# Optimization experiments

Hardware: AMD Instinct MI355X
Metric: run time of the kernel (lower is better)

The kernel has to match this reference:

```python
import jax, jax.numpy as jnp
import numpy as np

B, DIM, H, W = 8, 256, 128, 128
P = 4               # patch_size
HEADS = 8
HD = DIM // HEADS   # head dim = 32
CPB_HIDDEN = 512    # hidden width of the dynamic RPE MLP


def setup_inputs() -> dict:
    key = jax.random.key(0)
    ks = jax.random.split(key, 12)
    s = 0.02
    return {
        "x": jax.random.normal(ks[0], (B, DIM, H, W), dtype=jnp.float32),
        # PatchEmbed2d: Conv2d(dim, dim, kernel=P, stride=P)  weight [O, I, P, P]
        "w_embed": jax.random.normal(ks[1], (DIM, DIM, P, P), dtype=jnp.float32) * s,
        "b_embed": jnp.zeros((DIM,), dtype=jnp.float32),
        # DynamicPosEncoder: MLP(2 -> CPB_HIDDEN -> HEADS) on relative coords
        "cpb_w1": jax.random.normal(ks[2], (CPB_HIDDEN, 2), dtype=jnp.float32) * s,
        "cpb_b1": jnp.zeros((CPB_HIDDEN,), dtype=jnp.float32),
        "cpb_w2": jax.random.normal(ks[3], (HEADS, CPB_HIDDEN), dtype=jnp.float32) * s,
        # MaskAttention2d
        "w_qkv": jax.random.normal(ks[4], (3 * DIM, DIM), dtype=jnp.float32) * s,
        "b_qkv": jnp.zeros((3 * DIM,), dtype=jnp.float32),
        "w_proj": jax.random.normal(ks[5], (DIM, DIM), dtype=jnp.float32) * s,
        "b_proj": jnp.zeros((DIM,), dtype=jnp.float32),
        # PatchUnEmbed2d: ConvTranspose2d(dim, dim, kernel=P, stride=P)  weight [I, O, P, P]
        "w_unembed": jax.random.normal(ks[6], (DIM, DIM, P, P), dtype=jnp.float32) * s,
        "b_unembed": jnp.zeros((DIM,), dtype=jnp.float32),
    }


def _rpe_bias(Hp, Wp, cpb_w1, cpb_b1, cpb_w2):
    """Dynamic relative position bias -> [HEADS, N, N], N = Hp*Wp."""
    # continuous relative-coordinate table [(2Hp-1)*(2Wp-1), 2], normalized to [-1, 1]
    rh = (jnp.arange(2 * Hp - 1, dtype=jnp.float32) - (Hp - 1)) / max(Hp - 1, 1)
    rw = (jnp.arange(2 * Wp - 1, dtype=jnp.float32) - (Wp - 1)) / max(Wp - 1, 1)
    rel = jnp.stack(jnp.meshgrid(rh, rw, indexing="ij"), axis=-1).reshape(-1, 2)
    table = jax.nn.relu(rel @ cpb_w1.T + cpb_b1) @ cpb_w2.T  # [(2Hp-1)(2Wp-1), HEADS]
    # static relative position index [N, N]
    ch = np.arange(Hp)
    cw = np.arange(Wp)
    coords = np.stack(np.meshgrid(ch, cw, indexing="ij")).reshape(2, -1)  # [2, N]
    d = coords[:, :, None] - coords[:, None, :]                           # [2, N, N]
    idx = (d[0] + Hp - 1) * (2 * Wp - 1) + (d[1] + Wp - 1)               # [N, N]
    bias = table[jnp.asarray(idx)]                                        # [N, N, HEADS]
    return bias.transpose(2, 0, 1)                                        # [HEADS, N, N]


def reference(x, w_embed, b_embed, cpb_w1, cpb_b1, cpb_w2,
              w_qkv, b_qkv, w_proj, b_proj, w_unembed, b_unembed):
    Bx, C, Hf, Wf = x.shape
    Hp, Wp = Hf // P, Wf // P
    N = Hp * Wp
    # ---- patch embed: Conv2d(k=P, s=P) as block reshape + einsum ----
    xr = x.reshape(Bx, C, Hp, P, Wp, P)
    z = jnp.einsum("bchpwq,ocpq->bohw", xr, w_embed) + b_embed[None, :, None, None]
    # ---- dynamic RPE bias ----
    bias = _rpe_bias(Hp, Wp, cpb_w1, cpb_b1, cpb_w2)  # [HEADS, N, N]
    # ---- multi-head self-attention over the Hp*Wp grid ----
    tok = z.reshape(Bx, C, N).transpose(0, 2, 1)                     # [B, N, C]
    qkv = tok @ w_qkv.T + b_qkv                                       # [B, N, 3C]
    qkv = qkv.reshape(Bx, N, 3, HEADS, HD).transpose(2, 0, 3, 1, 4)   # [3, B, H, N, hd]
    q, k, v = qkv[0], qkv[1], qkv[2]
    scale = HD ** -0.5
    attn = jnp.einsum("bhnd,bhmd->bhnm", q * scale, k) + bias[None]   # [B, H, N, N]
    attn = jax.nn.softmax(attn, axis=-1)
    out = jnp.einsum("bhnm,bhmd->bhnd", attn, v)                      # [B, H, N, hd]
    out = out.transpose(0, 2, 1, 3).reshape(Bx, N, C)
    out = out @ w_proj.T + b_proj                                     # [B, N, C]
    z2 = out.transpose(0, 2, 1).reshape(Bx, C, Hp, Wp)
    # ---- patch unembed: ConvTranspose2d(k=P, s=P) as einsum + block reshape ----
    y = jnp.einsum("bchw,copq->bohpwq", z2, w_unembed)
    y = y.reshape(Bx, C, Hf, Wf) + b_unembed[None, :, None, None]
    return y
```

## Files before the change

kernel.cpp:

```cpp
#include <hip/hip_runtime.h>
#include <cstdint>
#include <cstddef>


typedef __bf16 bf16x8 __attribute__((ext_vector_type(8)));
typedef float f32x4 __attribute__((ext_vector_type(4)));
typedef unsigned short u16x4 __attribute__((ext_vector_type(4)));

__device__ __forceinline__ unsigned short f2bf(float f) {
  unsigned u = __builtin_bit_cast(unsigned, f);
  u += 0x7fffu + ((u >> 16) & 1u);
  return (unsigned short)(u >> 16);
}
__device__ __forceinline__ float bf2f(unsigned short u) {
  return __builtin_bit_cast(float, ((unsigned)u) << 16);
}

__device__ __forceinline__ void async_ld16(const void* g, void* l) {
  __builtin_amdgcn_global_load_lds(
      (const __attribute__((address_space(1))) void*)g,
      (__attribute__((address_space(3))) void*)l, 16, 0, 0);
}

__device__ __forceinline__ void cvt8_store(unsigned short* dst, float4 a,
                                           float4 b) {
  unsigned short t[8] = {f2bf(a.x), f2bf(a.y), f2bf(a.z), f2bf(a.w),
                         f2bf(b.x), f2bf(b.y), f2bf(b.z), f2bf(b.w)};
  *(uint4*)dst = *(const uint4*)t;
}

__global__ __launch_bounds__(256) void rpe_table_kernel(
    const float* __restrict__ w1, const float* __restrict__ b1,
    const float* __restrict__ w2, float* __restrict__ tableT) {
  int t = blockIdx.x * 256 + threadIdx.x;
  if (t >= 3969) return;
  int a = t / 63, c = t - a * 63;
  float rh = (float)(a - 31) * (1.0f / 31.0f);
  float rw = (float)(c - 31) * (1.0f / 31.0f);
  float acc[8];
#pragma unroll
  for (int h = 0; h < 8; h++) acc[h] = 0.f;
  for (int j = 0; j < 512; j++) {
    float hv = fmaxf(rh * w1[2 * j] + rw * w1[2 * j + 1] + b1[j], 0.f);
#pragma unroll
    for (int h = 0; h < 8; h++) acc[h] += hv * w2[h * 512 + j];
  }
#pragma unroll
  for (int h = 0; h < 8; h++) tableT[h * 4096 + t] = acc[h];
}

__global__ __launch_bounds__(256) void cvt_bf16_kernel(
    const float* __restrict__ src, unsigned short* __restrict__ dst, int n8) {
  int i = blockIdx.x * 256 + threadIdx.x;
  if (i >= n8) return;
  const float4* s4 = (const float4*)src + (size_t)i * 2;
  float4 a = s4[0], b = s4[1];
  unsigned short t[8] = {f2bf(a.x), f2bf(a.y), f2bf(a.z), f2bf(a.w),
                         f2bf(b.x), f2bf(b.y), f2bf(b.z), f2bf(b.w)};
  *(uint4*)(dst + (size_t)i * 8) = *(const uint4*)t;
}

__global__ __launch_bounds__(256) void transpose_cvt_kernel(
    const float* __restrict__ src, unsigned short* __restrict__ dst) {
  __shared__ float tile[32][33];
  int bx = blockIdx.x;
  int by = blockIdx.y;
  int tx = threadIdx.x & 31, ty = threadIdx.x >> 5;
#pragma unroll
  for (int r = 0; r < 32; r += 8)
    tile[ty + r][tx] = src[(size_t)(by * 32 + ty + r) * 4096 + bx * 32 + tx];
  __syncthreads();
#pragma unroll
  for (int r = 0; r < 32; r += 8)
    dst[(size_t)(bx * 32 + ty + r) * 256 + by * 32 + tx] = f2bf(tile[tx][ty + r]);
}

__global__ __launch_bounds__(256) void splitk_reduce_kernel(
    const float* __restrict__ part, const float* __restrict__ bias,
    unsigned short* __restrict__ out) {
  size_t i = ((size_t)blockIdx.x * 256 + threadIdx.x) * 8;
  const float4* p = (const float4*)(part + i);
  const size_t s4 = 2097152 / 4;
  float4 a0 = p[0], a1 = p[1];
#pragma unroll
  for (int s = 1; s < 4; s++) {
    float4 b0 = p[s * s4], b1 = p[s * s4 + 1];
    a0.x += b0.x; a0.y += b0.y; a0.z += b0.z; a0.w += b0.w;
    a1.x += b1.x; a1.y += b1.y; a1.z += b1.z; a1.w += b1.w;
  }
  int col = (int)(i & 255);
  unsigned short t8[8] = {
      f2bf(a0.x + bias[col + 0]), f2bf(a0.y + bias[col + 1]),
      f2bf(a0.z + bias[col + 2]), f2bf(a0.w + bias[col + 3]),
      f2bf(a1.x + bias[col + 4]), f2bf(a1.y + bias[col + 5]),
      f2bf(a1.z + bias[col + 6]), f2bf(a1.w + bias[col + 7])};
  *(uint4*)(out + i) = *(const uint4*)t8;
}

__global__ __launch_bounds__(256) void gemm_embed_kernel(
    const float* __restrict__ x, const unsigned short* __restrict__ B,
    float* __restrict__ Cpart) {
  __shared__ unsigned short As[2 * 128 * 32];
  __shared__ unsigned short Bs[2 * 128 * 32];
  int tid = threadIdx.x;
  int lane = tid & 63, wave = tid >> 6;

  int L = blockIdx.x;
  int xcd = L & 7, j = L >> 3;
  int pair = xcd * 32 + (j >> 1);
  int n0 = (j & 1) * 128;
  int z = pair & 3, y = pair >> 2;
  int m0 = y * 128;
  int wm = (wave & 1) * 64, wn = (wave >> 1) * 64;
  int fr = lane & 15, fh = lane >> 4;

  f32x4 acc[4][4];
#pragma unroll
  for (int i = 0; i < 4; i++)
#pragma unroll
    for (int jj = 0; jj < 4; jj++) acc[i][jj] = (f32x4){0.f, 0.f, 0.f, 0.f};

  int f0 = tid, f1 = tid + 256;
  const unsigned short* Bg0 =
      B + (size_t)(n0 + (f0 >> 2)) * 4096 + z * 1024 + (f0 & 3) * 8;
  const unsigned short* Bg1 =
      B + (size_t)(n0 + (f1 >> 2)) * 4096 + z * 1024 + (f1 & 3) * 8;
  unsigned short* Bl0 = Bs + f0 * 8;
  unsigned short* Bl1 = Bs + f1 * 8;

  const float4* x4 = (const float4*)x;
  int r0 = f0 >> 2, ch0 = f0 & 3;
  int m_0 = m0 + r0, b_0 = m_0 >> 10, hp0 = (m_0 >> 5) & 31, wp0 = m_0 & 31;
  int k_0 = z * 1024 + ch0 * 8, c_0 = k_0 >> 4, p_0 = (k_0 >> 2) & 3;
  const float4* xp0 =
      x4 + (size_t)((b_0 * 256 + c_0) * 128 + hp0 * 4 + p_0) * 32 + wp0;
  int r1 = f1 >> 2, ch1 = f1 & 3;
  int m_1 = m0 + r1, b_1 = m_1 >> 10, hp1 = (m_1 >> 5) & 31, wp1 = m_1 & 31;
  int k_1 = z * 1024 + ch1 * 8, c_1 = k_1 >> 4, p_1 = (k_1 >> 2) & 3;
  const float4* xp1 =
      x4 + (size_t)((b_1 * 256 + c_1) * 128 + hp1 * 4 + p_1) * 32 + wp1;
  unsigned short* Al0 = As + f0 * 8;
  unsigned short* Al1 = As + f1 * 8;

  float4 a00 = xp0[0], a01 = xp0[32], a10 = xp1[0], a11 = xp1[32];
  xp0 += 8192; xp1 += 8192;
  async_ld16(Bg0, Bl0);
  async_ld16(Bg1, Bl1);
  cvt8_store(Al0, a00, a01);
  cvt8_store(Al1, a10, a11);
  __syncthreads();

  for (int t = 0; t < 32; t++) {
    int cur = (t & 1) << 12, nxt = cur ^ 4096;
    if (t < 31) {
      a00 = xp0[0]; a01 = xp0[32]; a10 = xp1[0]; a11 = xp1[32];
      xp0 += 8192; xp1 += 8192;
      int kn = (t + 1) << 5;
      async_ld16(Bg0 + kn, Bl0 + nxt);
      async_ld16(Bg1 + kn, Bl1 + nxt);
    }
    const unsigned short* Asc = As + cur;
    const unsigned short* Bsc = Bs + cur;
    bf16x8 af[4], bfr[4];
#pragma unroll
    for (int tt = 0; tt < 4; tt++) {
      af[tt] = *(const bf16x8*)(Asc + (wm + tt * 16 + fr) * 32 + fh * 8);
      bfr[tt] = *(const bf16x8*)(Bsc + (wn + tt * 16 + fr) * 32 + fh * 8);
    }
#pragma unroll
    for (int mt = 0; mt < 4; mt++)
#pragma unroll
      for (int nt = 0; nt < 4; nt++)
        acc[mt][nt] = __builtin_amdgcn_mfma_f32_16x16x32_bf16(
            af[mt], bfr[nt], acc[mt][nt], 0, 0, 0);
    if (t < 31) {
      cvt8_store(Al0 + nxt, a00, a01);
      cvt8_store(Al1 + nxt, a10, a11);
    }
    __syncthreads();
  }

  float* Cp = Cpart + (size_t)z * 2097152;
#pragma unroll
  for (int mt = 0; mt < 4; mt++) {
    int row0 = m0 + wm + mt * 16 + fh * 4;
#pragma unroll
    for (int nt = 0; nt < 4; nt++) {
      int col = n0 + wn + nt * 16 + fr;
#pragma unroll
      for (int r = 0; r < 4; r++)
        Cp[(size_t)(row0 + r) * 256 + col] = acc[mt][nt][r];
    }
  }
}

template <int CMODE>
__global__ __launch_bounds__(256) void gemm_mfma_kernel(
    const unsigned short* __restrict__ A, const unsigned short* __restrict__ B,
    const float* __restrict__ bias, void* __restrict__ Cv,
    int M, int N, int K, int lda, int ldb, int ldc) {
  __shared__ unsigned short As[2 * 128 * 32];
  __shared__ unsigned short Bs[2 * 128 * 32];
  int tid = threadIdx.x;
  int lane = tid & 63;
  int wave = tid >> 6;
  int m0 = blockIdx.y * 128, n0 = blockIdx.x * 128;
  int wm = (wave & 1) * 64, wn = (wave >> 1) * 64;

  if (CMODE == 4) {
    int s = blockIdx.z;
    A += (size_t)s * K;
    B += (size_t)s * K;
    Cv = (void*)((float*)Cv + (size_t)s * M * N);
  }

  f32x4 acc[4][4];
#pragma unroll
  for (int i = 0; i < 4; i++)
#pragma unroll
    for (int j = 0; j < 4; j++) acc[i][j] = (f32x4){0.f, 0.f, 0.f, 0.f};

  int f0 = tid, f1 = tid + 256;
  const unsigned short* Ag0 = A + (size_t)(m0 + (f0 >> 2)) * lda + (f0 & 3) * 8;
  const unsigned short* Ag1 = A + (size_t)(m0 + (f1 >> 2)) * lda + (f1 & 3) * 8;
  const unsigned short* Bg0 = B + (size_t)(n0 + (f0 >> 2)) * ldb + (f0 & 3) * 8;
  const unsigned short* Bg1 = B + (size_t)(n0 + (f1 >> 2)) * ldb + (f1 & 3) * 8;
  unsigned short* Al0 = As + f0 * 8;
  unsigned short* Al1 = As + f1 * 8;
  unsigned short* Bl0 = Bs + f0 * 8;
  unsigned short* Bl1 = Bs + f1 * 8;

  int fr = lane & 15;
  int fh = lane >> 4;

  int ntiles = K >> 5;
  async_ld16(Ag0, Al0);
  async_ld16(Ag1, Al1);
  async_ld16(Bg0, Bl0);
  async_ld16(Bg1, Bl1);
  __syncthreads();

  for (int t = 0; t < ntiles; t++) {
    int cur = (t & 1) << 12;
    int nxt = cur ^ 4096;
    if (t + 1 < ntiles) {
      int kn = (t + 1) << 5;
      async_ld16(Ag0 + kn, Al0 + nxt);
      async_ld16(Ag1 + kn, Al1 + nxt);
      async_ld16(Bg0 + kn, Bl0 + nxt);
      async_ld16(Bg1 + kn, Bl1 + nxt);
    }
    const unsigned short* Asc = As + cur;
    const unsigned short* Bsc = Bs + cur;
    bf16x8 af[4], bfr[4];
#pragma unroll
    for (int tt = 0; tt < 4; tt++) {
      af[tt] = *(const bf16x8*)(Asc + (wm + tt * 16 + fr) * 32 + fh * 8);
      bfr[tt] = *(const bf16x8*)(Bsc + (wn + tt * 16 + fr) * 32 + fh * 8);
    }
#pragma unroll
    for (int mt = 0; mt < 4; mt++)
#pragma unroll
      for (int nt = 0; nt < 4; nt++)
        acc[mt][nt] = __builtin_amdgcn_mfma_f32_16x16x32_bf16(
            af[mt], bfr[nt], acc[mt][nt], 0, 0, 0);
    __syncthreads();
  }

#pragma unroll
  for (int mt = 0; mt < 4; mt++) {
    int row0 = m0 + wm + mt * 16 + fh * 4;
    if (CMODE == 2) {
      int b = row0 >> 10, hp = (row0 >> 5) & 31, wp = row0 & 31;
      size_t rowoff0 = (size_t)b * 4194304 + hp * 512 + wp * 4;
      float* y = (float*)Cv;
#pragma unroll
      for (int nt = 0; nt < 4; nt++) {
        int col = n0 + wn + nt * 16 + fr;
        int o = col >> 4, p = (col >> 2) & 3, q = col & 3;
        size_t coloff = (size_t)o * 16384 + p * 128 + q;
        float bv = bias[o];
#pragma unroll
        for (int r = 0; r < 4; r++)
          y[rowoff0 + r * 4 + coloff] = acc[mt][nt][r] + bv;
      }
    } else if (CMODE == 3) {
      unsigned short* base = (unsigned short*)Cv;
#pragma unroll
      for (int nt = 0; nt < 4; nt++) {
        int col = n0 + wn + nt * 16 + fr;
        int which = col >> 8, hh = (col >> 5) & 7, d = col & 31;
        float bv = bias[col];
#pragma unroll
        for (int r = 0; r < 4; r++) {
          int row = row0 + r;
          int bb = row >> 10, nn = row & 1023;
          int bh = bb * 8 + hh;
          float v = acc[mt][nt][r] + bv;
          if (which == 0) v *= 0.17677669529663687f;
          size_t addr;
          if (which < 2)
            addr = (size_t)which * 2097152 + ((size_t)bh * 1024 + nn) * 32 + d;
          else
            addr = (size_t)2 * 2097152 + (size_t)bh * 32768 + (size_t)d * 1024 + nn;
          base[addr] = f2bf(v);
        }
      }
    } else if (CMODE == 4) {
      float* Cp = (float*)Cv;
#pragma unroll
      for (int nt = 0; nt < 4; nt++) {
        int col = n0 + wn + nt * 16 + fr;
#pragma unroll
        for (int r = 0; r < 4; r++)
          Cp[(size_t)(row0 + r) * ldc + col] = acc[mt][nt][r];
      }
    } else {
#pragma unroll
      for (int nt = 0; nt < 4; nt++) {
        int col = n0 + wn + nt * 16 + fr;
        float bv = bias ? bias[col] : 0.f;
        unsigned short* C = (unsigned short*)Cv;
#pragma unroll
        for (int r = 0; r < 4; r++)
          C[(size_t)(row0 + r) * ldc + col] = f2bf(acc[mt][nt][r] + bv);
      }
    }
  }
}

__global__ __launch_bounds__(512) void attn_mfma_kernel(
    const unsigned short* __restrict__ Qb, const unsigned short* __restrict__ Kb,
    const unsigned short* __restrict__ Vtb,
    const float* __restrict__ tableT,
    unsigned short* __restrict__ out) {
  __shared__ float th[3972];
  __shared__ unsigned short Ps[2][8][1088];

  int tid = threadIdx.x;
  int lane = tid & 63, w = tid >> 6;
  int n = lane & 15, g = lane >> 4;
  int blk = blockIdx.x;
  int h = blk & 7, b = (blk >> 3) & 7, qt = blk >> 6;
  int bh = b * 8 + h;
  int q0 = qt * 128;

  const unsigned short* Qg = Qb + ((size_t)bh * 1024 + q0) * 32;
  const unsigned short* Kg = Kb + (size_t)bh * 1024 * 32;
  const unsigned short* Vg = Vtb + (size_t)bh * 32 * 1024;
  const float* tg = tableT + (size_t)h * 4096;

  for (int i = tid; i < 3969; i += 512) th[i] = tg[i];
  bf16x8 qf = *(const bf16x8*)(Qg + (size_t)(w * 16 + n) * 32 + g * 8);
  __syncthreads();

  f32x4 oacc[2];
  oacc[0] = (f32x4){0.f, 0.f, 0.f, 0.f};
  oacc[1] = (f32x4){0.f, 0.f, 0.f, 0.f};
  float m_run = -1e30f, l_run = 0.f;

  int q = q0 + w * 16 + n;
  int tbase = (q >> 5) * 63 + (q & 31) + 1984;

  unsigned short* PwA = &Ps[0][w][0];
  unsigned short* PwB = &Ps[1][w][0];

  bf16x8 kfA[4], kfB[4];
#pragma unroll
  for (int mt = 0; mt < 4; mt++)
    kfA[mt] = *(const bf16x8*)(Kg + (size_t)(mt * 16 + n) * 32 + g * 8);

  auto half_step = [&](const bf16x8 (&kf)[4], int k0, unsigned short* Pw) {
    bf16x8 vf[4];
#pragma unroll
    for (int i = 0; i < 4; i++)
      vf[i] = *(const bf16x8*)(Vg + (size_t)((i & 1) * 16 + n) * 1024 + k0 +
                               (i >> 1) * 32 + g * 8);

    f32x4 s[4];
    __builtin_amdgcn_s_setprio(1);
#pragma unroll
    for (int mt = 0; mt < 4; mt++)
      s[mt] = __builtin_amdgcn_mfma_f32_16x16x32_bf16(
          kf[mt], qf, (f32x4){0.f, 0.f, 0.f, 0.f}, 0, 0, 0);
    __builtin_amdgcn_s_setprio(0);

#pragma unroll
    for (int mt = 0; mt < 4; mt++) {
      int kb = k0 + mt * 16 + g * 4;
      int ib = tbase - (kb >> 5) * 63 - (kb & 31);
      s[mt][0] += th[ib];
      s[mt][1] += th[ib - 1];
      s[mt][2] += th[ib - 2];
      s[mt][3] += th[ib - 3];
    }

    float mx = -1e30f;
#pragma unroll
    for (int mt = 0; mt < 4; mt++)
#pragma unroll
      for (int r = 0; r < 4; r++) mx = fmaxf(mx, s[mt][r]);
    mx = fmaxf(mx, __shfl_xor(mx, 16, 64));
    mx = fmaxf(mx, __shfl_xor(mx, 32, 64));
    float m_new = fmaxf(m_run, mx);
    float alpha = __expf(m_run - m_new);
    m_run = m_new;

    float ls = 0.f;
#pragma unroll
    for (int mt = 0; mt < 4; mt++) {
#pragma unroll
      for (int r = 0; r < 4; r++) {
        float p = __expf(s[mt][r] - m_new);
        s[mt][r] = p;
        ls += p;
      }
      u16x4 pk = {f2bf(s[mt][0]), f2bf(s[mt][1]), f2bf(s[mt][2]),
                  f2bf(s[mt][3])};
      *(u16x4*)(Pw + n * 68 + mt * 16 + g * 4) = pk;
    }
    l_run = l_run * alpha + ls;

#pragma unroll
    for (int dt = 0; dt < 2; dt++)
#pragma unroll
      for (int r = 0; r < 4; r++) oacc[dt][r] *= alpha;
    __builtin_amdgcn_s_setprio(1);
#pragma unroll
    for (int kt = 0; kt < 2; kt++) {
      bf16x8 pf = *(const bf16x8*)(Pw + n * 68 + kt * 32 + g * 8);
      oacc[0] = __builtin_amdgcn_mfma_f32_16x16x32_bf16(vf[kt * 2 + 0], pf,
                                                        oacc[0], 0, 0, 0);
      oacc[1] = __builtin_amdgcn_mfma_f32_16x16x32_bf16(vf[kt * 2 + 1], pf,
                                                        oacc[1], 0, 0, 0);
    }
    __builtin_amdgcn_s_setprio(0);
  };

  for (int tt = 0; tt < 8; tt++) {
    int k0 = tt * 128;
#pragma unroll
    for (int mt = 0; mt < 4; mt++)
      kfB[mt] = *(const bf16x8*)(Kg + (size_t)(k0 + 64 + mt * 16 + n) * 32 +
                                 g * 8);
    half_step(kfA, k0, PwA);
    if (tt < 7) {
#pragma unroll
      for (int mt = 0; mt < 4; mt++)
        kfA[mt] = *(const bf16x8*)(Kg + (size_t)(k0 + 128 + mt * 16 + n) * 32 +
                                   g * 8);
    }
    half_step(kfB, k0 + 64, PwB);
  }

  float l = l_run;
  l += __shfl_xor(l, 16, 64);
  l += __shfl_xor(l, 32, 64);
  float invl = 1.f / l;
  unsigned short* ob = out + ((size_t)(b * 1024 + q) * 256) + h * 32;
#pragma unroll
  for (int dt = 0; dt < 2; dt++) {
    u16x4 o4 = {f2bf(oacc[dt][0] * invl), f2bf(oacc[dt][1] * invl),
                f2bf(oacc[dt][2] * invl), f2bf(oacc[dt][3] * invl)};
    *(u16x4*)(ob + dt * 16 + g * 4) = o4;
  }
}

extern "C" void kernel_launch(void* const* d_in, const int* in_sizes, int n_in,
                              void* d_out, int out_size, void* d_ws, size_t ws_size,
                              hipStream_t stream) {
  const float* x         = (const float*)d_in[0];
  const float* w_embed   = (const float*)d_in[1];
  const float* b_embed   = (const float*)d_in[2];
  const float* cpb_w1    = (const float*)d_in[3];
  const float* cpb_b1    = (const float*)d_in[4];
  const float* cpb_w2    = (const float*)d_in[5];
  const float* w_qkv     = (const float*)d_in[6];
  const float* b_qkv     = (const float*)d_in[7];
  const float* w_proj    = (const float*)d_in[8];
  const float* b_proj    = (const float*)d_in[9];
  const float* w_unembed = (const float*)d_in[10];
  const float* b_unembed = (const float*)d_in[11];
  float* out = (float*)d_out;

  char* w = (char*)d_ws;
  float*          ProjP = (float*)w;          w += (size_t)8388608 * 4;
  unsigned short* tok   = (unsigned short*)w; w += (size_t)8192 * 256 * 2;
  unsigned short* wE    = (unsigned short*)w; w += (size_t)1048576 * 2;
  unsigned short* wQ    = (unsigned short*)w; w += (size_t)196608 * 2;
  unsigned short* wP    = (unsigned short*)w; w += (size_t)65536 * 2;
  unsigned short* wUt   = (unsigned short*)w; w += (size_t)1048576 * 2;
  float*          tableT= (float*)w;          w += (size_t)32768 * 4;
  float*          PART  = (float*)w;          w += (size_t)8388608 * 4;

  unsigned short* qkvB  = (unsigned short*)PART;
  unsigned short* attno = (unsigned short*)((char*)PART + 12582912);
  unsigned short* z2    = (unsigned short*)((char*)PART + 16777216);
  unsigned short* Qb  = qkvB;
  unsigned short* Kb  = qkvB + 2097152;
  unsigned short* Vtb = qkvB + 2 * 2097152;

  cvt_bf16_kernel<<<512, 256, 0, stream>>>(w_embed, wE, 131072);
  cvt_bf16_kernel<<<96, 256, 0, stream>>>(w_qkv, wQ, 24576);
  cvt_bf16_kernel<<<32, 256, 0, stream>>>(w_proj, wP, 8192);
  transpose_cvt_kernel<<<dim3(128, 8), 256, 0, stream>>>(w_unembed, wUt);
  rpe_table_kernel<<<16, 256, 0, stream>>>(cpb_w1, cpb_b1, cpb_w2, tableT);

  gemm_embed_kernel<<<512, 256, 0, stream>>>(x, wE, PART);
  splitk_reduce_kernel<<<1024, 256, 0, stream>>>(PART, b_embed, tok);

  gemm_mfma_kernel<3><<<dim3(6, 64), 256, 0, stream>>>(
      tok, wQ, b_qkv, qkvB, 8192, 768, 256, 256, 256, 0);

  attn_mfma_kernel<<<512, 512, 0, stream>>>(Qb, Kb, Vtb, tableT, attno);

  gemm_mfma_kernel<4><<<dim3(2, 64, 4), 256, 0, stream>>>(
      attno, wP, nullptr, ProjP, 8192, 256, 64, 256, 256, 256);
  splitk_reduce_kernel<<<1024, 256, 0, stream>>>(ProjP, b_proj, z2);

  gemm_mfma_kernel<2><<<dim3(32, 64), 256, 0, stream>>>(
      z2, wUt, b_unembed, out, 8192, 4096, 256, 256, 256, 0);
}
```

Before: 496.1 us.

## Load embed GEMM fragments directly from global into registers, dropping LDS

The patch-embed GEMM no longer stages A and B tiles through shared memory with barriers. Each lane now loads its own MFMA fragments straight from global memory into registers, converts fp32 to bf16 in registers, and ping-pongs two register sets to overlap loads with MFMAs. It also raises MFMA priority and sets launch bounds to 2 blocks per CU. This removes LDS traffic and __syncthreads, but each wave now re-reads data other waves also need, so global and L2 traffic rise, and register pressure grows.

New measurement: 494.1 us. About the same (-0.4%).

```diff
diff --git a/kernel.cpp b/kernel.cpp
--- a/kernel.cpp
+++ b/kernel.cpp
@@ -22,11 +22,10 @@
       (__attribute__((address_space(3))) void*)l, 16, 0, 0);
 }
 
-__device__ __forceinline__ void cvt8_store(unsigned short* dst, float4 a,
-                                           float4 b) {
+__device__ __forceinline__ bf16x8 cvt8f(float4 a, float4 b) {
   unsigned short t[8] = {f2bf(a.x), f2bf(a.y), f2bf(a.z), f2bf(a.w),
                          f2bf(b.x), f2bf(b.y), f2bf(b.z), f2bf(b.w)};
-  *(uint4*)dst = *(const uint4*)t;
+  return *(const bf16x8*)t;
 }
 
 __global__ __launch_bounds__(256) void rpe_table_kernel(
@@ -97,11 +96,9 @@
   *(uint4*)(out + i) = *(const uint4*)t8;
 }
 
-__global__ __launch_bounds__(256) void gemm_embed_kernel(
+__global__ __launch_bounds__(256, 2) void gemm_embed_kernel(
     const float* __restrict__ x, const unsigned short* __restrict__ B,
     float* __restrict__ Cpart) {
-  __shared__ unsigned short As[2 * 128 * 32];
-  __shared__ unsigned short Bs[2 * 128 * 32];
   int tid = threadIdx.x;
   int lane = tid & 63, wave = tid >> 6;
 
@@ -120,65 +117,57 @@
 #pragma unroll
     for (int jj = 0; jj < 4; jj++) acc[i][jj] = (f32x4){0.f, 0.f, 0.f, 0.f};
 
-  int f0 = tid, f1 = tid + 256;
-  const unsigned short* Bg0 =
-      B + (size_t)(n0 + (f0 >> 2)) * 4096 + z * 1024 + (f0 & 3) * 8;
-  const unsigned short* Bg1 =
-      B + (size_t)(n0 + (f1 >> 2)) * 4096 + z * 1024 + (f1 & 3) * 8;
-  unsigned short* Bl0 = Bs + f0 * 8;
-  unsigned short* Bl1 = Bs + f1 * 8;
-
   const float4* x4 = (const float4*)x;
-  int r0 = f0 >> 2, ch0 = f0 & 3;
-  int m_0 = m0 + r0, b_0 = m_0 >> 10, hp0 = (m_0 >> 5) & 31, wp0 = m_0 & 31;
-  int k_0 = z * 1024 + ch0 * 8, c_0 = k_0 >> 4, p_0 = (k_0 >> 2) & 3;
-  const float4* xp0 =
-      x4 + (size_t)((b_0 * 256 + c_0) * 128 + hp0 * 4 + p_0) * 32 + wp0;
-  int r1 = f1 >> 2, ch1 = f1 & 3;
-  int m_1 = m0 + r1, b_1 = m_1 >> 10, hp1 = (m_1 >> 5) & 31, wp1 = m_1 & 31;
-  int k_1 = z * 1024 + ch1 * 8, c_1 = k_1 >> 4, p_1 = (k_1 >> 2) & 3;
-  const float4* xp1 =
-      x4 + (size_t)((b_1 * 256 + c_1) * 128 + hp1 * 4 + p_1) * 32 + wp1;
-  unsigned short* Al0 = As + f0 * 8;
-  unsigned short* Al1 = As + f1 * 8;
-
-  float4 a00 = xp0[0], a01 = xp0[32], a10 = xp1[0], a11 = xp1[32];
-  xp0 += 8192; xp1 += 8192;
-  async_ld16(Bg0, Bl0);
-  async_ld16(Bg1, Bl1);
-  cvt8_store(Al0, a00, a01);
-  cvt8_store(Al1, a10, a11);
-  __syncthreads();
-
-  for (int t = 0; t < 32; t++) {
-    int cur = (t & 1) << 12, nxt = cur ^ 4096;
-    if (t < 31) {
-      a00 = xp0[0]; a01 = xp0[32]; a10 = xp1[0]; a11 = xp1[32];
-      xp0 += 8192; xp1 += 8192;
-      int kn = (t + 1) << 5;
-      async_ld16(Bg0 + kn, Bl0 + nxt);
-      async_ld16(Bg1 + kn, Bl1 + nxt);
-    }
-    const unsigned short* Asc = As + cur;
-    const unsigned short* Bsc = Bs + cur;
-    bf16x8 af[4], bfr[4];
-#pragma unroll
-    for (int tt = 0; tt < 4; tt++) {
-      af[tt] = *(const bf16x8*)(Asc + (wm + tt * 16 + fr) * 32 + fh * 8);
-      bfr[tt] = *(const bf16x8*)(Bsc + (wn + tt * 16 + fr) * 32 + fh * 8);
-    }
+  int c0 = z * 64 + (fh >> 1);
+  int p0 = (fh * 2) & 3;
+  const float4* xp[4];
+#pragma unroll
+  for (int tt = 0; tt < 4; tt++) {
+    int m = m0 + wm + tt * 16 + fr;
+    int b_ = m >> 10, hp = (m >> 5) & 31, wp = m & 31;
+    xp[tt] = x4 + (size_t)((b_ * 256 + c0) * 128 + hp * 4 + p0) * 32 + wp;
+  }
+  const unsigned short* bp[4];
+#pragma unroll
+  for (int tt = 0; tt < 4; tt++)
+    bp[tt] = B + (size_t)(n0 + wn + tt * 16 + fr) * 4096 + z * 1024 + fh * 8;
+
+  float4 aA[8], aB[8];
+  bf16x8 bA[4], bB[4];
+
+#define LOADF(areg, breg, AOFF, BOFF)                  \
+  {                                                    \
+    _Pragma("unroll") for (int tt = 0; tt < 4; tt++) { \
+      areg[2 * tt] = xp[tt][AOFF];                     \
+      areg[2 * tt + 1] = xp[tt][AOFF + 32];            \
+      breg[tt] = *(const bf16x8*)(bp[tt] + BOFF);      \
+    }                                                  \
+  }
+
+  auto compute = [&](float4 (&a)[8], bf16x8 (&bfr)[4]) {
+    bf16x8 af[4];
+#pragma unroll
+    for (int tt = 0; tt < 4; tt++) af[tt] = cvt8f(a[2 * tt], a[2 * tt + 1]);
+    __builtin_amdgcn_s_setprio(1);
 #pragma unroll
     for (int mt = 0; mt < 4; mt++)
 #pragma unroll
       for (int nt = 0; nt < 4; nt++)
         acc[mt][nt] = __builtin_amdgcn_mfma_f32_16x16x32_bf16(
             af[mt], bfr[nt], acc[mt][nt], 0, 0, 0);
-    if (t < 31) {
-      cvt8_store(Al0 + nxt, a00, a01);
-      cvt8_store(Al1 + nxt, a10, a11);
-    }
-    __syncthreads();
-  }
+    __builtin_amdgcn_s_setprio(0);
+  };
+
+  LOADF(aA, bA, 0, 0);
+  for (int it = 0; it < 16; it++) {
+    LOADF(aB, bB, 8192, 32);
+    compute(aA, bA);
+    if (it < 15) LOADF(aA, bA, 16384, 64);
+    compute(aB, bB);
+#pragma unroll
+    for (int tt = 0; tt < 4; tt++) { xp[tt] += 16384; bp[tt] += 64; }
+  }
+#undef LOADF
 
   float* Cp = Cpart + (size_t)z * 2097152;
 #pragma unroll
```
